# Performance work log

Measured on AMD Instinct MI355X. Metric: run time of the kernel, lower is better.

## Reference

```python
import jax, jax.numpy as jnp
import numpy as np

DIM = 1024
HEADS = 16
DIM_HEAD = 64
INNER = HEADS * DIM_HEAD
SCALE = DIM_HEAD ** -0.5


def rotate_half(t):
    # '... (j d) -> ... j d' with j=2: split last dim in half
    x1, x2 = jnp.split(t, 2, axis=-1)
    return jnp.concatenate((-x2, x1), axis=-1)


def rotary_pos(n, d, dtype):
    inv_freq = 1.0 / (10000.0 ** (jnp.arange(0, d, 2, dtype=jnp.float32) / d))
    freqs = jnp.arange(n, dtype=jnp.float32)[:, None] * inv_freq[None, :]  # (n, d/2)
    return jnp.concatenate((freqs, freqs), axis=-1).astype(dtype)  # (n, d)


def apply_rope(pos, t):
    return t * jnp.cos(pos) + rotate_half(t) * jnp.sin(pos)


def setup_inputs() -> dict:
    key = jax.random.key(0)
    ks = jax.random.split(key, 5)
    x = jax.random.normal(ks[0], (2, 2048, DIM), dtype=jnp.float32)
    gamma = jnp.ones((DIM,), dtype=jnp.float32)
    beta = jnp.zeros((DIM,), dtype=jnp.float32)
    Wq = jax.random.normal(ks[1], (DIM, INNER), dtype=jnp.float32) * 0.02
    Wkv = jax.random.normal(ks[2], (DIM, 2 * INNER), dtype=jnp.float32) * 0.02
    Wo = jax.random.normal(ks[3], (INNER, DIM), dtype=jnp.float32) * 0.02
    return {"x": x, "gamma": gamma, "beta": beta, "Wq": Wq, "Wkv": Wkv, "Wo": Wo}


def reference(x, gamma, beta, Wq, Wkv, Wo):
    b, n, _ = x.shape
    # LayerNorm with learned gamma, fixed-zero beta buffer
    mu = jnp.mean(x, axis=-1, keepdims=True)
    var = jnp.var(x, axis=-1, keepdims=True)
    xn = (x - mu) / jnp.sqrt(var + 1e-5) * gamma + beta

    q = xn @ Wq                       # (b, n, inner)
    kv = xn @ Wkv
    k, v = jnp.split(kv, 2, axis=-1)

    def to_heads(t):
        return t.reshape(b, n, HEADS, DIM_HEAD).transpose(0, 2, 1, 3)  # b h n d

    q, k, v = map(to_heads, (q, k, v))

    pos = rotary_pos(n, DIM_HEAD, x.dtype)  # (n, d)
    q = apply_rope(pos, q)
    k = apply_rope(pos, k)

    q = q * SCALE
    sim = jnp.einsum('bhid,bhjd->bhij', q, k)

    neg = -jnp.finfo(sim.dtype).max
    causal_mask = jnp.triu(jnp.ones((n, n), dtype=bool), k=1)
    sim = jnp.where(causal_mask, neg, sim)

    attn = jax.nn.softmax(sim, axis=-1)
    out = jnp.einsum('bhij,bhjd->bhid', attn, v)
    out = out.transpose(0, 2, 1, 3).reshape(b, n, INNER)
    return out @ Wo
```

## Files before the change

kernel.cpp:

```cpp
#include <hip/hip_runtime.h>
#include <stdint.h>

typedef unsigned short u16;
typedef __attribute__((ext_vector_type(8))) short short8;
typedef __attribute__((ext_vector_type(4))) float floatx4;
typedef __attribute__((ext_vector_type(4))) unsigned short u16x4;
typedef __attribute__((ext_vector_type(2))) unsigned int uint2v;

__device__ __forceinline__ float bf2f(u16 v) {
  union { uint32_t u; float f; } x; x.u = ((uint32_t)v) << 16; return x.f;
}
__device__ __forceinline__ u16 f2bf(float f) {
  union { float f; uint32_t u; } x; x.f = f;
  uint32_t r = x.u + 0x7fffu + ((x.u >> 16) & 1u);
  return (u16)(r >> 16);
}
__device__ __forceinline__ uint32_t fu(float f) {
  union { float f; uint32_t u; } x; x.f = f; return x.u;
}

#define GL2LDS(g, l)                                                          \
  __builtin_amdgcn_global_load_lds(                                           \
      (const __attribute__((address_space(1))) void*)(g),                     \
      (__attribute__((address_space(3))) void*)(l), 16, 0, 0)

#define WAITBAR(N)                                                            \
  asm volatile("s_waitcnt vmcnt(" #N ")\n\ts_barrier" ::: "memory")
#define BARX asm volatile("s_barrier" ::: "memory")
#define VM0BARX asm volatile("s_waitcnt vmcnt(0)\n\ts_barrier" ::: "memory")

__device__ __forceinline__ void xcd_remap(int bid, int& bmi, int& bni) {
  int x = bid & 7, s = bid >> 3;
  bmi = ((x >> 1) << 3) | (s & 7);
  bni = ((x & 1) << 2) | (s >> 3);
}

__global__ __launch_bounds__(256) void prep_k(const float* __restrict__ x,
                                              const float* __restrict__ gamma,
                                              const float* __restrict__ beta,
                                              const float* __restrict__ Wq,
                                              const float* __restrict__ Wkv,
                                              const float* __restrict__ Wo,
                                              u16* __restrict__ xn,
                                              u16* __restrict__ wqkvT,
                                              u16* __restrict__ woT) {
  int bid = blockIdx.x;
  int t = threadIdx.x;
  if (bid < 4096) {
    int row = bid;
    const float* xr = x + (size_t)row * 1024;
    float4 xv = *(const float4*)(xr + t * 4);
    float v0 = xv.x, v1 = xv.y, v2 = xv.z, v3 = xv.w;
    float s = v0 + v1 + v2 + v3;
    float s2 = v0 * v0 + v1 * v1 + v2 * v2 + v3 * v3;
#pragma unroll
    for (int d = 1; d < 64; d <<= 1) {
      s += __shfl_xor(s, d, 64);
      s2 += __shfl_xor(s2, d, 64);
    }
    __shared__ float red[8];
    int lane = t & 63, wv = t >> 6;
    if (lane == 0) { red[wv] = s; red[4 + wv] = s2; }
    __syncthreads();
    s = red[0] + red[1] + red[2] + red[3];
    s2 = red[4] + red[5] + red[6] + red[7];
    float mu = s * (1.0f / 1024.0f);
    float var = s2 * (1.0f / 1024.0f) - mu * mu;
    float rstd = rsqrtf(var + 1e-5f);
    float4 gv = *(const float4*)(gamma + t * 4);
    float4 bv = *(const float4*)(beta + t * 4);
    u16x4 ov;
    ov.x = f2bf((v0 - mu) * rstd * gv.x + bv.x);
    ov.y = f2bf((v1 - mu) * rstd * gv.y + bv.y);
    ov.z = f2bf((v2 - mu) * rstd * gv.z + bv.z);
    ov.w = f2bf((v3 - mu) * rstd * gv.w + bv.w);
    *(u16x4*)(xn + (size_t)row * 1024 + t * 4) = ov;
  } else {
    __shared__ u16 ldst[64][72];
    int wb = bid - 4096;
    const float* in;
    u16* outp;
    int C;
    if (wb < 256) { in = Wq; outp = wqkvT; C = 1024; }
    else if (wb < 768) { wb -= 256; in = Wkv; outp = wqkvT + 1024 * 1024; C = 2048; }
    else { wb -= 768; in = Wo; outp = woT; C = 1024; }
    int nbx = C >> 6;
    int c0 = (wb % nbx) * 64, r0 = (wb / nbx) * 64;
    int rt = t >> 2;
    int ci = (t & 3) * 16;
    const float* ip = in + (size_t)(r0 + rt) * C + c0 + ci;
#pragma unroll
    for (int q = 0; q < 4; q++) {
      float4 v = *(const float4*)(ip + q * 4);
      ldst[ci + q * 4 + 0][rt] = f2bf(v.x);
      ldst[ci + q * 4 + 1][rt] = f2bf(v.y);
      ldst[ci + q * 4 + 2][rt] = f2bf(v.z);
      ldst[ci + q * 4 + 3][rt] = f2bf(v.w);
    }
    __syncthreads();
    int ct = t >> 2;
    int ri = (t & 3) * 16;
    u16* op = outp + (size_t)(c0 + ct) * 1024 + r0 + ri;
    *(short8*)(op) = *(const short8*)&ldst[ct][ri];
    *(short8*)(op + 8) = *(const short8*)&ldst[ct][ri + 8];
  }
}

__global__ __launch_bounds__(512, 1) void gemm_qkv_k(const u16* __restrict__ A,
                                                     const u16* __restrict__ BT,
                                                     u16* __restrict__ C) {
  __shared__ __align__(16) u16 sA[2][128 * 64];
  __shared__ __align__(16) u16 sB[2][384 * 64];
  int tid = threadIdx.x;
  int w = tid >> 6, l = tid & 63;
  int lr = l & 15, lq = l >> 4;
  int wm = w >> 1, wn = w & 1;
  int bmi, bni;
  xcd_remap(blockIdx.x, bmi, bni);
  int bm = bmi * 128;
  int bn = bni * 384;
  floatx4 acc[2][12] = {};
  int gcol = ((tid & 7) ^ ((tid >> 3) & 7)) * 8;
  int strow = tid >> 3;
  int t8 = tid * 8;
  const u16* gA = A + (size_t)(bm + strow) * 1024 + gcol;
  const u16* gB = BT + (size_t)(bn + strow) * 1024 + gcol;
  int csw = (lr & 7) << 3;
  int ar = (wm * 32 + lr) * 64;
  int br = (wn * 192 + lr) * 64;

#define ST_A(bi)                                                              \
  { GL2LDS(gA, &sA[bi][t8]); GL2LDS(gA + 65536, &sA[bi][t8 + 4096]); }
#define ST_B(bi)                                                              \
  { GL2LDS(gB, &sB[bi][t8]);                                                  \
    GL2LDS(gB + 65536, &sB[bi][t8 + 4096]);                                   \
    GL2LDS(gB + 131072, &sB[bi][t8 + 8192]);                                  \
    GL2LDS(gB + 196608, &sB[bi][t8 + 12288]);                                 \
    GL2LDS(gB + 262144, &sB[bi][t8 + 16384]);                                 \
    GL2LDS(gB + 327680, &sB[bi][t8 + 20480]); }
#define HALF(p, kh)                                                           \
  {                                                                           \
    int co_ = ((kh)*32 + lq * 8) ^ csw;                                       \
    short8 a0_ = *(const short8*)&sA[p][ar + co_];                            \
    short8 a1_ = *(const short8*)&sA[p][ar + 1024 + co_];                     \
    _Pragma("unroll") for (int g = 0; g < 3; g++) {                           \
      short8 b0_ = *(const short8*)&sB[p][br + (g * 4 + 0) * 1024 + co_];     \
      short8 b1_ = *(const short8*)&sB[p][br + (g * 4 + 1) * 1024 + co_];     \
      short8 b2_ = *(const short8*)&sB[p][br + (g * 4 + 2) * 1024 + co_];     \
      short8 b3_ = *(const short8*)&sB[p][br + (g * 4 + 3) * 1024 + co_];     \
      acc[0][g*4+0] = __builtin_amdgcn_mfma_f32_16x16x32_bf16(a0_, b0_, acc[0][g*4+0], 0, 0, 0); \
      acc[1][g*4+0] = __builtin_amdgcn_mfma_f32_16x16x32_bf16(a1_, b0_, acc[1][g*4+0], 0, 0, 0); \
      acc[0][g*4+1] = __builtin_amdgcn_mfma_f32_16x16x32_bf16(a0_, b1_, acc[0][g*4+1], 0, 0, 0); \
      acc[1][g*4+1] = __builtin_amdgcn_mfma_f32_16x16x32_bf16(a1_, b1_, acc[1][g*4+1], 0, 0, 0); \
      acc[0][g*4+2] = __builtin_amdgcn_mfma_f32_16x16x32_bf16(a0_, b2_, acc[0][g*4+2], 0, 0, 0); \
      acc[1][g*4+2] = __builtin_amdgcn_mfma_f32_16x16x32_bf16(a1_, b2_, acc[1][g*4+2], 0, 0, 0); \
      acc[0][g*4+3] = __builtin_amdgcn_mfma_f32_16x16x32_bf16(a0_, b3_, acc[0][g*4+3], 0, 0, 0); \
      acc[1][g*4+3] = __builtin_amdgcn_mfma_f32_16x16x32_bf16(a1_, b3_, acc[1][g*4+3], 0, 0, 0); \
    }                                                                         \
  }
#define KT(p, q, DOST)                                                        \
  {                                                                           \
    if (DOST) { ST_A(q); ST_B(q); gA += 64; gB += 64; }                       \
    BARX; __builtin_amdgcn_s_setprio(1);                                      \
    HALF(p, 0);                                                               \
    __builtin_amdgcn_s_setprio(0); BARX;                                      \
    __builtin_amdgcn_s_setprio(1);                                            \
    HALF(p, 1);                                                               \
    __builtin_amdgcn_s_setprio(0); VM0BARX;                                   \
  }

  ST_A(0); ST_B(0); gA += 64; gB += 64;
  VM0BARX;
#pragma unroll 1
  for (int t = 0; t < 7; ++t) {
    KT(0, 1, 1);
    KT(1, 0, 1);
  }
  KT(0, 1, 1);
  KT(1, 0, 0);

#pragma unroll
  for (int nig = 0; nig < 3; nig++) {
    int col0 = bn + wn * 192 + nig * 64;
    int sec = col0 >> 10;
    if (sec == 2) {
#pragma unroll
      for (int p4 = 0; p4 < 4; p4++) {
        int ni = nig * 4 + p4;
        int col = col0 + p4 * 16 + lr;
        int cv = col - 2048;
#pragma unroll
        for (int mi = 0; mi < 2; mi++) {
          int row = bm + wm * 32 + mi * 16 + lq * 4;
          int bq = row >> 11;
          int n = row & 2047;
          int bh = (bq << 4) | (cv >> 6);
          int d = cv & 63;
          size_t L = ((size_t)(bh * 64 + d) << 11) + n;
          u16x4 ov;
          ov.x = f2bf(acc[mi][ni][0]);
          ov.y = f2bf(acc[mi][ni][1]);
          ov.z = f2bf(acc[mi][ni][2]);
          ov.w = f2bf(acc[mi][ni][3]);
          *(u16x4*)(C + (L >> 10) * 3072 + 2048 + (L & 1023)) = ov;
        }
      }
    } else {
      float QS = (sec == 0) ? 0.125f * 1.44269504088896f : 1.0f;
#pragma unroll
      for (int np = 0; np < 2; np++) {
        int i = np * 16 + lr;
        float invf = exp2f(-(float)i * 0.4152410118609203f);
#pragma unroll
        for (int mi = 0; mi < 2; mi++)
#pragma unroll
          for (int r = 0; r < 4; r++) {
            int row = bm + wm * 32 + mi * 16 + lq * 4 + r;
            int n = row & 2047;
            float ang = (float)n * invf;
            float s_, c_;
            __sincosf(ang, &s_, &c_);
            float x1 = acc[mi][nig * 4 + np][r];
            float x2 = acc[mi][nig * 4 + np + 2][r];
            int col = col0 + np * 16 + lr;
            C[(size_t)row * 3072 + col] = f2bf((x1 * c_ - x2 * s_) * QS);
            C[(size_t)row * 3072 + col + 32] = f2bf((x2 * c_ + x1 * s_) * QS);
          }
      }
    }
  }
}

__global__ __launch_bounds__(512, 1) void gemm64_bf16_k(const u16* __restrict__ A,
                                                        const u16* __restrict__ BT,
                                                        float* __restrict__ C) {
  __shared__ __align__(16) u16 sA[2][128 * 64];
  __shared__ __align__(16) u16 sB[2][128 * 64];
  int tid = threadIdx.x;
  int w = tid >> 6, l = tid & 63;
  int lr = l & 15, lq = l >> 4;
  int wm = w >> 1, wn = w & 1;
  int bmi, bni;
  xcd_remap(blockIdx.x, bmi, bni);
  int bm = bmi * 128;
  int bn = bni * 128;
  floatx4 acc[2][4] = {};
  int gcol = ((tid & 7) ^ ((tid >> 3) & 7)) * 8;
  int strow = tid >> 3;
  int t8 = tid * 8;
  const u16* gA = A + (size_t)(bm + strow) * 1024 + gcol;
  const u16* gB = BT + (size_t)(bn + strow) * 1024 + gcol;
  int csw = (lr & 7) << 3;
  int ar = (wm * 32 + lr) * 64;
  int br = (wn * 64 + lr) * 64;

#define ST_A2(bi)                                                             \
  { GL2LDS(gA, &sA[bi][t8]); GL2LDS(gA + 65536, &sA[bi][t8 + 4096]); }
#define ST_B2(bi)                                                             \
  { GL2LDS(gB, &sB[bi][t8]); GL2LDS(gB + 65536, &sB[bi][t8 + 4096]); }
#define HALF2(p, kh)                                                          \
  {                                                                           \
    int co_ = ((kh)*32 + lq * 8) ^ csw;                                       \
    short8 a0_ = *(const short8*)&sA[p][ar + co_];                            \
    short8 a1_ = *(const short8*)&sA[p][ar + 1024 + co_];                     \
    short8 b0_ = *(const short8*)&sB[p][br + 0 + co_];                        \
    short8 b1_ = *(const short8*)&sB[p][br + 1024 + co_];                     \
    short8 b2_ = *(const short8*)&sB[p][br + 2048 + co_];                     \
    short8 b3_ = *(const short8*)&sB[p][br + 3072 + co_];                     \
    acc[0][0] = __builtin_amdgcn_mfma_f32_16x16x32_bf16(a0_, b0_, acc[0][0], 0, 0, 0); \
    acc[1][0] = __builtin_amdgcn_mfma_f32_16x16x32_bf16(a1_, b0_, acc[1][0], 0, 0, 0); \
    acc[0][1] = __builtin_amdgcn_mfma_f32_16x16x32_bf16(a0_, b1_, acc[0][1], 0, 0, 0); \
    acc[1][1] = __builtin_amdgcn_mfma_f32_16x16x32_bf16(a1_, b1_, acc[1][1], 0, 0, 0); \
    acc[0][2] = __builtin_amdgcn_mfma_f32_16x16x32_bf16(a0_, b2_, acc[0][2], 0, 0, 0); \
    acc[1][2] = __builtin_amdgcn_mfma_f32_16x16x32_bf16(a1_, b2_, acc[1][2], 0, 0, 0); \
    acc[0][3] = __builtin_amdgcn_mfma_f32_16x16x32_bf16(a0_, b3_, acc[0][3], 0, 0, 0); \
    acc[1][3] = __builtin_amdgcn_mfma_f32_16x16x32_bf16(a1_, b3_, acc[1][3], 0, 0, 0); \
  }
#define KT2(p, q, DOST)                                                       \
  {                                                                           \
    if (DOST) { ST_A2(q); ST_B2(q); gA += 64; gB += 64; }                     \
    BARX; __builtin_amdgcn_s_setprio(1);                                      \
    HALF2(p, 0);                                                              \
    __builtin_amdgcn_s_setprio(0); BARX;                                      \
    __builtin_amdgcn_s_setprio(1);                                            \
    HALF2(p, 1);                                                              \
    __builtin_amdgcn_s_setprio(0); VM0BARX;                                   \
  }

  ST_A2(0); ST_B2(0); gA += 64; gB += 64;
  VM0BARX;
#pragma unroll 1
  for (int t = 0; t < 7; ++t) {
    KT2(0, 1, 1);
    KT2(1, 0, 1);
  }
  KT2(0, 1, 1);
  KT2(1, 0, 0);

#pragma unroll
  for (int mi = 0; mi < 2; mi++)
#pragma unroll
    for (int ni = 0; ni < 4; ni++) {
      int row = bm + wm * 32 + mi * 16 + lq * 4;
      int col = bn + wn * 64 + ni * 16 + lr;
#pragma unroll
      for (int r = 0; r < 4; r++)
        C[(size_t)(row + r) * 1024 + col] = acc[mi][ni][r];
    }
}

#define LPT 64
__device__ __forceinline__ void attn_tile2(const u16* lK, const u16* lV, u16* lp,
                                           const short8* aq, floatx4* o,
                                           float& l_i, int lr, int lq,
                                           bool diag, int q0, int k0g) {
  floatx4 s[4];
#pragma unroll
  for (int ni = 0; ni < 4; ni++) {
    floatx4 a = {};
#pragma unroll
    for (int kc = 0; kc < 2; kc++) {
      int R = ni * 16 + lr;
      int c8 = (kc * 4 + lq) ^ (R & 7);
      short8 kf = *(const short8*)&lK[R * 64 + c8 * 8];
      a = __builtin_amdgcn_mfma_f32_16x16x32_bf16(kf, aq[kc], a, 0, 0, 0);
    }
    s[ni] = a;
  }
  if (diag) {
    int qg = q0 + lr;
#pragma unroll
    for (int ni = 0; ni < 4; ni++)
#pragma unroll
      for (int r = 0; r < 4; r++) {
        int kg = k0g + ni * 16 + lq * 4 + r;
        if (kg > qg) s[ni][r] = -1e30f;
      }
  }
  int swz = (lr & 7) << 3;
#pragma unroll
  for (int ni = 0; ni < 4; ni++) {
    float p0 = exp2f(s[ni][0]), p1 = exp2f(s[ni][1]);
    float p2 = exp2f(s[ni][2]), p3 = exp2f(s[ni][3]);
    l_i += (p0 + p1) + (p2 + p3);
    uint2v dw;
    dw.x = __builtin_amdgcn_perm(fu(p1), fu(p0), 0x07060302u);
    dw.y = __builtin_amdgcn_perm(fu(p3), fu(p2), 0x07060302u);
    *(uint2v*)&lp[lr * LPT + ((ni * 16 + lq * 4) ^ swz)] = dw;
  }
  short8 pb0 = *(const short8*)&lp[lr * LPT + ((lq * 8) ^ swz)];
  short8 pb1 = *(const short8*)&lp[lr * LPT + ((32 + lq * 8) ^ swz)];
#pragma unroll
  for (int di = 0; di < 4; di++) {
    int R = di * 16 + lr;
    int c80 = lq ^ (R & 7);
    int c81 = (4 + lq) ^ (R & 7);
    short8 v0 = *(const short8*)&lV[R * 64 + c80 * 8];
    o[di] = __builtin_amdgcn_mfma_f32_16x16x32_bf16(v0, pb0, o[di], 0, 0, 0);
    short8 v1 = *(const short8*)&lV[R * 64 + c81 * 8];
    o[di] = __builtin_amdgcn_mfma_f32_16x16x32_bf16(v1, pb1, o[di], 0, 0, 0);
  }
}

__global__ __launch_bounds__(256) void attn_k(const u16* __restrict__ qkv,
                                              u16* __restrict__ out) {
  __shared__ __align__(16) u16 lK[2][64 * 64];
  __shared__ __align__(16) u16 lV[2][64 * 64];
  __shared__ __align__(16) u16 lP[4][16 * LPT];
  int bh = blockIdx.x;
  int b = bh >> 4, h = bh & 15;
  int y = blockIdx.y;
  int g = y >> 3, o_ = y & 7;
  int j = (g & 1) ? ((g << 3) + 7 - o_) : y;
  int tid = threadIdx.x;
  int w = tid >> 6, l = tid & 63;
  int lr = l & 15, lq = l >> 4;
  int q0 = j * 64 + w * 16;
  const u16* qb = qkv + (size_t)b * 2048 * 3072 + h * 64;
  const u16* kb = qkv + (size_t)b * 2048 * 3072 + 1024 + h * 64;
  int bh64 = bh * 64;
  short8 aq[2];
  aq[0] = *(const short8*)(qb + (size_t)(q0 + lr) * 3072 + lq * 8);
  aq[1] = *(const short8*)(qb + (size_t)(q0 + lr) * 3072 + 32 + lq * 8);
  floatx4 o[4] = {};
  float l_ = 0.0f;
  int srow8 = l >> 3;
  int sc8 = (l & 7) ^ srow8;
  u16* lp = &lP[w][0];
  int row0 = w * 8 + srow8;
  int row1 = (w + 4) * 8 + srow8;
  const u16* kp0 = kb + (size_t)row0 * 3072 + sc8 * 8;
  const u16* kp1 = kb + (size_t)row1 * 3072 + sc8 * 8;
  const u16* vp0 = qkv + (size_t)((bh64 + row0) * 2) * 3072 + 2048 + sc8 * 8;
  const u16* vp1 = qkv + (size_t)((bh64 + row1) * 2) * 3072 + 2048 + sc8 * 8;
  auto stage = [&](int bufi) {
    GL2LDS(kp0, &lK[bufi][w * 512]);
    GL2LDS(vp0, &lV[bufi][w * 512]);
    GL2LDS(kp1, &lK[bufi][(w + 4) * 512]);
    GL2LDS(vp1, &lV[bufi][(w + 4) * 512]);
  };
  auto advance = [&](int ktStaged) {
    kp0 += 196608; kp1 += 196608;
    int dv = (((ktStaged + 1) & 15) == 0) ? 2112 : 64;
    vp0 += dv; vp1 += dv;
  };
  stage(0);
  advance(0);
  for (int kt = 0; kt <= j; ++kt) {
    int cur = kt & 1;
    __syncthreads();
    if (kt < j) { stage(cur ^ 1); advance(kt + 1); }
    attn_tile2(lK[cur], lV[cur], lp, aq, o, l_, lr, lq, kt == j, q0, kt * 64);
  }
  l_ += __shfl_xor(l_, 16, 64);
  l_ += __shfl_xor(l_, 32, 64);
  float rl = 1.0f / l_;
#pragma unroll
  for (int di = 0; di < 4; di++) {
    uint2v dw;
    u16 a0 = f2bf(o[di][0] * rl), a1 = f2bf(o[di][1] * rl);
    u16 a2 = f2bf(o[di][2] * rl), a3 = f2bf(o[di][3] * rl);
    dw.x = (uint32_t)a0 | ((uint32_t)a1 << 16);
    dw.y = (uint32_t)a2 | ((uint32_t)a3 << 16);
    int dcol = h * 64 + di * 16 + lq * 4;
    *(uint2v*)(out + ((size_t)(b * 2048 + q0 + lr)) * 1024 + dcol) = dw;
  }
}

extern "C" void kernel_launch(void* const* d_in, const int* in_sizes, int n_in,
                              void* d_out, int out_size, void* d_ws, size_t ws_size,
                              hipStream_t stream) {
  const float* x = (const float*)d_in[0];
  const float* gamma = (const float*)d_in[1];
  const float* beta = (const float*)d_in[2];
  const float* Wq = (const float*)d_in[3];
  const float* Wkv = (const float*)d_in[4];
  const float* Wo = (const float*)d_in[5];
  float* out = (float*)d_out;
  char* ws = (char*)d_ws;

  u16* qkv = (u16*)(ws);
  u16* wqkvT = (u16*)(ws + 25165824);
  u16* woT = (u16*)(ws + 31457280);
  u16* xn = (u16*)(ws + 33554432);
  u16* attn_out = xn;

  prep_k<<<5120, 256, 0, stream>>>(x, gamma, beta, Wq, Wkv, Wo, xn, wqkvT, woT);
  gemm_qkv_k<<<256, 512, 0, stream>>>(xn, wqkvT, qkv);
  attn_k<<<dim3(32, 32), 256, 0, stream>>>(qkv, attn_out);
  gemm64_bf16_k<<<256, 512, 0, stream>>>(attn_out, woT, out);
}
```

Baseline: 178.9 us.

## Triple-buffer QKV GEMM with 32-wide K stages; compute softmax row sums via MFMA

The QKV projection GEMM moves from a double-buffered 64-wide K tile with two barriers per tile to a three-stage ring of 32-wide K tiles. Each stage is issued two steps ahead and guarded by a partial vmcnt wait, so global-to-LDS loads overlap more with MFMA work. This uses a new swizzle for the narrower LDS rows. Separately, the attention kernel now gets the softmax denominator from an MFMA of a ones vector against the bf16 probabilities, replacing the scalar adds and the final cross-lane shuffles, which also makes the normalizer use the same rounded values as P·V.

```diff
diff --git a/kernel.cpp b/kernel.cpp
--- a/kernel.cpp
+++ b/kernel.cpp
@@ -109,8 +109,8 @@
 __global__ __launch_bounds__(512, 1) void gemm_qkv_k(const u16* __restrict__ A,
                                                      const u16* __restrict__ BT,
                                                      u16* __restrict__ C) {
-  __shared__ __align__(16) u16 sA[2][128 * 64];
-  __shared__ __align__(16) u16 sB[2][384 * 64];
+  __shared__ __align__(16) u16 sA[3][128 * 32];
+  __shared__ __align__(16) u16 sB[3][384 * 32];
   int tid = threadIdx.x;
   int w = tid >> 6, l = tid & 63;
   int lr = l & 15, lq = l >> 4;
@@ -120,34 +120,31 @@
   int bm = bmi * 128;
   int bn = bni * 384;
   floatx4 acc[2][12] = {};
-  int gcol = ((tid & 7) ^ ((tid >> 3) & 7)) * 8;
-  int strow = tid >> 3;
+  int strow = tid >> 2;
+  int gcol = ((tid & 3) ^ ((tid >> 3) & 3)) * 8;
   int t8 = tid * 8;
   const u16* gA = A + (size_t)(bm + strow) * 1024 + gcol;
   const u16* gB = BT + (size_t)(bn + strow) * 1024 + gcol;
-  int csw = (lr & 7) << 3;
-  int ar = (wm * 32 + lr) * 64;
-  int br = (wn * 192 + lr) * 64;
-
-#define ST_A(bi)                                                              \
-  { GL2LDS(gA, &sA[bi][t8]); GL2LDS(gA + 65536, &sA[bi][t8 + 4096]); }
-#define ST_B(bi)                                                              \
-  { GL2LDS(gB, &sB[bi][t8]);                                                  \
-    GL2LDS(gB + 65536, &sB[bi][t8 + 4096]);                                   \
-    GL2LDS(gB + 131072, &sB[bi][t8 + 8192]);                                  \
-    GL2LDS(gB + 196608, &sB[bi][t8 + 12288]);                                 \
-    GL2LDS(gB + 262144, &sB[bi][t8 + 16384]);                                 \
-    GL2LDS(gB + 327680, &sB[bi][t8 + 20480]); }
-#define HALF(p, kh)                                                           \
+  int rs = (lq ^ ((lr >> 1) & 3)) * 8;
+  int ar0 = (wm * 32 + lr) * 32 + rs;
+  int br0 = (wn * 192 + lr) * 32 + rs;
+
+#define ST32(bi)                                                              \
+  { GL2LDS(gA, &sA[bi][t8]);                                                  \
+    GL2LDS(gB, &sB[bi][t8]);                                                  \
+    GL2LDS(gB + 131072, &sB[bi][t8 + 4096]);                                  \
+    GL2LDS(gB + 262144, &sB[bi][t8 + 8192]);                                  \
+    gA += 32; gB += 32; }
+#define COMP32(bi)                                                            \
   {                                                                           \
-    int co_ = ((kh)*32 + lq * 8) ^ csw;                                       \
-    short8 a0_ = *(const short8*)&sA[p][ar + co_];                            \
-    short8 a1_ = *(const short8*)&sA[p][ar + 1024 + co_];                     \
+    short8 a0_ = *(const short8*)&sA[bi][ar0];                                \
+    short8 a1_ = *(const short8*)&sA[bi][ar0 + 512];                          \
+    __builtin_amdgcn_s_setprio(1);                                            \
     _Pragma("unroll") for (int g = 0; g < 3; g++) {                           \
-      short8 b0_ = *(const short8*)&sB[p][br + (g * 4 + 0) * 1024 + co_];     \
-      short8 b1_ = *(const short8*)&sB[p][br + (g * 4 + 1) * 1024 + co_];     \
-      short8 b2_ = *(const short8*)&sB[p][br + (g * 4 + 2) * 1024 + co_];     \
-      short8 b3_ = *(const short8*)&sB[p][br + (g * 4 + 3) * 1024 + co_];     \
+      short8 b0_ = *(const short8*)&sB[bi][br0 + (g * 4 + 0) * 512];          \
+      short8 b1_ = *(const short8*)&sB[bi][br0 + (g * 4 + 1) * 512];          \
+      short8 b2_ = *(const short8*)&sB[bi][br0 + (g * 4 + 2) * 512];          \
+      short8 b3_ = *(const short8*)&sB[bi][br0 + (g * 4 + 3) * 512];          \
       acc[0][g*4+0] = __builtin_amdgcn_mfma_f32_16x16x32_bf16(a0_, b0_, acc[0][g*4+0], 0, 0, 0); \
       acc[1][g*4+0] = __builtin_amdgcn_mfma_f32_16x16x32_bf16(a1_, b0_, acc[1][g*4+0], 0, 0, 0); \
       acc[0][g*4+1] = __builtin_amdgcn_mfma_f32_16x16x32_bf16(a0_, b1_, acc[0][g*4+1], 0, 0, 0); \
@@ -157,27 +154,19 @@
       acc[0][g*4+3] = __builtin_amdgcn_mfma_f32_16x16x32_bf16(a0_, b3_, acc[0][g*4+3], 0, 0, 0); \
       acc[1][g*4+3] = __builtin_amdgcn_mfma_f32_16x16x32_bf16(a1_, b3_, acc[1][g*4+3], 0, 0, 0); \
     }                                                                         \
-  }
-#define KT(p, q, DOST)                                                        \
-  {                                                                           \
-    if (DOST) { ST_A(q); ST_B(q); gA += 64; gB += 64; }                       \
-    BARX; __builtin_amdgcn_s_setprio(1);                                      \
-    HALF(p, 0);                                                               \
-    __builtin_amdgcn_s_setprio(0); BARX;                                      \
-    __builtin_amdgcn_s_setprio(1);                                            \
-    HALF(p, 1);                                                               \
-    __builtin_amdgcn_s_setprio(0); VM0BARX;                                   \
-  }
-
-  ST_A(0); ST_B(0); gA += 64; gB += 64;
-  VM0BARX;
+    __builtin_amdgcn_s_setprio(0);                                            \
+  }
+
+  ST32(0);
+  ST32(1);
 #pragma unroll 1
-  for (int t = 0; t < 7; ++t) {
-    KT(0, 1, 1);
-    KT(1, 0, 1);
-  }
-  KT(0, 1, 1);
-  KT(1, 0, 0);
+  for (int t = 0; t < 10; ++t) {
+    WAITBAR(4); ST32(2); COMP32(0);
+    WAITBAR(4); ST32(0); COMP32(1);
+    WAITBAR(4); ST32(1); COMP32(2);
+  }
+  WAITBAR(4); COMP32(0);
+  WAITBAR(0); COMP32(1);
 
 #pragma unroll
   for (int nig = 0; nig < 3; nig++) {
@@ -313,7 +302,8 @@
 __device__ __forceinline__ void attn_tile2(const u16* lK, const u16* lV, u16* lp,
                                            const short8* aq, floatx4* o,
                                            float& l_i, int lr, int lq,
-                                           bool diag, int q0, int k0g) {
+                                           bool diag, int q0, int k0g,
+                                           short8 ones) {
   floatx4 s[4];
 #pragma unroll
   for (int ni = 0; ni < 4; ni++) {
@@ -342,7 +332,6 @@
   for (int ni = 0; ni < 4; ni++) {
     float p0 = exp2f(s[ni][0]), p1 = exp2f(s[ni][1]);
     float p2 = exp2f(s[ni][2]), p3 = exp2f(s[ni][3]);
-    l_i += (p0 + p1) + (p2 + p3);
     uint2v dw;
     dw.x = __builtin_amdgcn_perm(fu(p1), fu(p0), 0x07060302u);
     dw.y = __builtin_amdgcn_perm(fu(p3), fu(p2), 0x07060302u);
@@ -350,6 +339,10 @@
   }
   short8 pb0 = *(const short8*)&lp[lr * LPT + ((lq * 8) ^ swz)];
   short8 pb1 = *(const short8*)&lp[lr * LPT + ((32 + lq * 8) ^ swz)];
+  floatx4 z = {};
+  z = __builtin_amdgcn_mfma_f32_16x16x32_bf16(ones, pb0, z, 0, 0, 0);
+  z = __builtin_amdgcn_mfma_f32_16x16x32_bf16(ones, pb1, z, 0, 0, 0);
+  l_i += z[0];
 #pragma unroll
   for (int di = 0; di < 4; di++) {
     int R = di * 16 + lr;
@@ -382,6 +375,9 @@
   short8 aq[2];
   aq[0] = *(const short8*)(qb + (size_t)(q0 + lr) * 3072 + lq * 8);
   aq[1] = *(const short8*)(qb + (size_t)(q0 + lr) * 3072 + 32 + lq * 8);
+  short8 ones;
+#pragma unroll
+  for (int i = 0; i < 8; i++) ones[i] = (short)0x3F80;
   floatx4 o[4] = {};
   float l_ = 0.0f;
   int srow8 = l >> 3;
@@ -410,10 +406,9 @@
     int cur = kt & 1;
     __syncthreads();
     if (kt < j) { stage(cur ^ 1); advance(kt + 1); }
-    attn_tile2(lK[cur], lV[cur], lp, aq, o, l_, lr, lq, kt == j, q0, kt * 64);
-  }
-  l_ += __shfl_xor(l_, 16, 64);
-  l_ += __shfl_xor(l_, 32, 64);
+    attn_tile2(lK[cur], lV[cur], lp, aq, o, l_, lr, lq, kt == j, q0, kt * 64,
+               ones);
+  }
   float rl = 1.0f / l_;
 #pragma unroll
   for (int di = 0; di < 4; di++) {
```

Result: no change. 182.4 us (+2.0%).
